# Kernel tuning notes

Measured on AMD Instinct MI355X. Metric: run time of the kernel, lower is better.

Reference implementation:

```python
import jax, jax.numpy as jnp
import numpy as np

G, P = 512, 128            # graphs, nodes per graph
NT, NL, NC = 120, 4, 4     # tracks/leptons/cells per graph (disjoint node targets)
W_NODE, W_BCE, W_F1 = 1.0, 1.0, 1.0  # config['loss weights']


def setup_inputs() -> dict:
    key = jax.random.key(0)
    ks = jax.random.split(key, 8)
    N = G * P
    T, L, C = G * NT, G * NL, G * NC
    E = G * P * P
    local = np.arange(P)[None, :] + (np.arange(G)[:, None] * P)  # [G,P] global node ids
    track_dst = jnp.asarray(local[:, :NT].ravel(), jnp.int32)
    lep_dst = jnp.asarray(local[:, NT:NT + NL].ravel(), jnp.int32)
    cell_dst = jnp.asarray(local[:, NT + NL:].ravel(), jnp.int32)
    ii, jj = np.meshgrid(np.arange(P), np.arange(P), indexing='ij')
    off = (np.arange(G) * P)[:, None, None]
    edge_src = jnp.asarray((off + ii[None]).reshape(-1), jnp.int32)
    edge_dst = jnp.asarray((off + jj[None]).reshape(-1), jnp.int32)
    edge_gid = jnp.asarray(np.repeat(np.arange(G), P * P), jnp.int32)
    node_gid = jnp.asarray(np.repeat(np.arange(G), P), jnp.int32)
    return {
        'node_prediction': jax.random.normal(ks[0], (N, 5), jnp.float32),
        'edge_prediction': jax.random.normal(ks[1], (E,), jnp.float32),
        'ce_weight': jnp.ones((5,), jnp.float32),
        'track_labels': jax.random.randint(ks[2], (T,), 0, 5, jnp.int32),
        'track_vtx': jax.random.randint(ks[3], (T,), 0, 10, jnp.int32),
        'lep_labels': jax.random.randint(ks[4], (L,), 0, 5, jnp.int32),
        'lep_vtx': jax.random.randint(ks[5], (L,), 0, 10, jnp.int32),
        'cell_labels': jax.random.randint(ks[6], (C,), 0, 5, jnp.int32),
        'cell_vtx': jax.random.randint(ks[7], (C,), 0, 10, jnp.int32),
        'track_dst': track_dst,
        'lep_dst': lep_dst,
        'cell_dst': cell_dst,
        'edge_src': edge_src,
        'edge_dst': edge_dst,
        'edge_gid': edge_gid,
        'node_gid': node_gid,
    }


def reference(node_prediction, edge_prediction, ce_weight,
              track_labels, track_vtx, lep_labels, lep_vtx, cell_labels, cell_vtx,
              track_dst, lep_dst, cell_dst, edge_src, edge_dst, edge_gid, node_gid):
    N = node_prediction.shape[0]

    def scatter(track_v, lep_v, cell_v):  # copy_src + sum over 3 edge types
        out = jnp.zeros((N,), jnp.int32)
        out = out.at[track_dst].add(track_v)
        out = out.at[lep_dst].add(lep_v)
        out = out.at[cell_dst].add(cell_v)
        return out

    node_labels = scatter(track_labels, lep_labels, cell_labels)
    node_vtx = scatter(track_vtx, lep_vtx, cell_vtx)

    # node CrossEntropyLoss (weight=[1]*5, ignore_index=-1, reduction='none')
    logp = jax.nn.log_softmax(node_prediction, axis=-1)
    valid = node_labels != -1
    lab = jnp.clip(node_labels, 0, 4)
    ce = -jnp.take_along_axis(logp, lab[:, None], axis=-1)[:, 0] * ce_weight[lab]
    ce = jnp.where(valid, ce, 0.0)
    node_loss = jax.ops.segment_sum(ce, node_gid, num_segments=G).mean()

    # edge weights (EdgeWeightFunction) and labels (EdgeLabelFunction)
    src_lab = node_labels[edge_src]
    dst_lab = node_labels[edge_dst]
    cond = ((dst_lab == 3) | (dst_lab == 2)) & ((src_lab == 3) | (src_lab == 2))
    w = jnp.where(cond, 2.0, 1.0).astype(jnp.float32)
    y = (node_vtx[edge_src] == node_vtx[edge_dst]).astype(jnp.float32)

    x = edge_prediction
    # BCEWithLogits: log(1+e^x) - x*y
    bce = (jnp.logaddexp(0.0, x) - x * y) * w
    e_cnt = jax.ops.segment_sum(jnp.ones_like(x), edge_gid, num_segments=G)
    edge_bce = (jax.ops.segment_sum(bce, edge_gid, num_segments=G) / e_cnt).mean()

    yh = jax.nn.sigmoid(x)
    tp = jax.ops.segment_sum(yh * y * w, edge_gid, num_segments=G)
    fn = jax.ops.segment_sum((1.0 - yh) * y * w, edge_gid, num_segments=G)
    fp = jax.ops.segment_sum(yh * (1.0 - y) * w, edge_gid, num_segments=G)
    edge_f1 = -(2.0 * tp / (2.0 * tp + fp + fn + 1e-10)).mean()

    loss = node_loss * W_NODE + edge_bce * W_BCE + edge_f1 * W_F1
    return loss
```

## Files before the change

### kernel.cpp

```cpp
#include <hip/hip_runtime.h>
#include <math.h>

#define NG     512
#define NP     128
#define NTRK   120
#define NLEP   4
#define NCEL   4
#define EPG    (NP * NP)
#define NTHREADS 256
#define SPLIT  4
#define NBLK   (NG * SPLIT)
#define EPB    (EPG / SPLIT)
#define F4ITERS (EPB / (NTHREADS * 4))


__global__ __launch_bounds__(NTHREADS) void vfl_main(
    const float* __restrict__ node_pred,
    const float* __restrict__ edge_pred,
    const float* __restrict__ ce_weight,
    const int* __restrict__ track_labels, const int* __restrict__ track_vtx,
    const int* __restrict__ lep_labels,   const int* __restrict__ lep_vtx,
    const int* __restrict__ cell_labels,  const int* __restrict__ cell_vtx,
    float* __restrict__ gout)
{
    const int b = blockIdx.x;
    const int g = b >> 2;
    const int s = b & 3;
    const int t = threadIdx.x;

    __shared__ float s_edge[EPB];
    __shared__ int   s_pack[NP];
    __shared__ float s_red[4][4];
    __shared__ int   s_cnt[10][2];

    {
        const float* ep_base = edge_pred + (size_t)g * EPG + (size_t)s * EPB;
        const int wv = t >> 6;
        const int ln = t & 63;
        #pragma unroll
        for (int k = 0; k < 4; ++k) {
            const int c = (k << 2) + wv;
            const float* gsrc = ep_base + c * 256 + ln * 4;
            __builtin_amdgcn_global_load_lds(
                (const __attribute__((address_space(1))) void*)gsrc,
                (__attribute__((address_space(3))) void*)&s_edge[c * 256],
                16, 0, 0);
        }
    }

    if (t < 20) ((int*)s_cnt)[t] = 0;

    float ce = 0.0f;
    int vtx = 0, is23 = 0;
    if (t < NP) {
        int lab;
        if (t < NTRK) {
            lab = track_labels[g * NTRK + t];
            vtx = track_vtx  [g * NTRK + t];
        } else if (t < NTRK + NLEP) {
            const int u = t - NTRK;
            lab = lep_labels[g * NLEP + u];
            vtx = lep_vtx  [g * NLEP + u];
        } else {
            const int u = t - NTRK - NLEP;
            lab = cell_labels[g * NCEL + u];
            vtx = cell_vtx  [g * NCEL + u];
        }
        is23 = (lab == 2 || lab == 3) ? 1 : 0;
        s_pack[t] = (vtx & 0xff) | (is23 << 8);

        if ((t >> 5) == s) {
            const float* np = node_pred + (size_t)(g * NP + t) * 5;
            const float x0 = np[0], x1 = np[1], x2 = np[2], x3 = np[3], x4 = np[4];
            const float m  = fmaxf(fmaxf(fmaxf(x0, x1), fmaxf(x2, x3)), x4);
            const float sm = __expf(x0 - m) + __expf(x1 - m) + __expf(x2 - m)
                           + __expf(x3 - m) + __expf(x4 - m);
            const float lse = m + __logf(sm);
            const float xl = (lab == 0) ? x0 : (lab == 1) ? x1 : (lab == 2) ? x2
                           : (lab == 3) ? x3 : x4;
            ce = (lse - xl) * ce_weight[lab];
        }
    }

    asm volatile("s_waitcnt vmcnt(0)" ::: "memory");
    __syncthreads();

    if (s == 0 && t < NP) atomicAdd(&s_cnt[vtx][is23], 1);

    const int j0 = (t & 31) << 2;
    const int pj0 = s_pack[j0 + 0];
    const int pj1 = s_pack[j0 + 1];
    const int pj2 = s_pack[j0 + 2];
    const int pj3 = s_pack[j0 + 3];
    const int ibase = s * 32 + (t >> 5);

    const float4* se4 = (const float4*)s_edge;

    float bce = 0.0f, swyh = 0.0f, tp = 0.0f;

    #pragma unroll
    for (int k = 0; k < F4ITERS; ++k) {
        const float4 v  = se4[k * NTHREADS + t];
        const int    pi = s_pack[ibase + k * 8];

        const float xs[4]  = { v.x, v.y, v.z, v.w };
        const int   pjs[4] = { pj0, pj1, pj2, pj3 };
        #pragma unroll
        for (int c = 0; c < 4; ++c) {
            const float x   = xs[c];
            const int   pjc = pjs[c];
            const bool  same = (((pi ^ pjc) & 0xff) == 0);
            const float w   = ((pi & pjc) & 0x100) ? 2.0f : 1.0f;
            const float wf  = same ? w : 0.0f;
            const float e  = __expf(-fabsf(x));
            const float t1 = 1.0f + e;
            const float r  = __builtin_amdgcn_rcpf(t1);
            const float sp = fmaxf(x, 0.0f) + __logf(t1);
            const float yh = (x >= 0.0f) ? r : (1.0f - r);
            bce  = fmaf(w,  sp, bce);
            bce  = fmaf(wf, -x, bce);
            swyh = fmaf(w,  yh, swyh);
            tp   = fmaf(wf, yh, tp);
        }
    }

    float vals[4] = { ce, bce, swyh, tp };
    #pragma unroll
    for (int i = 0; i < 4; ++i) {
        float x = vals[i];
        #pragma unroll
        for (int off = 32; off > 0; off >>= 1)
            x += __shfl_xor(x, off, 64);
        vals[i] = x;
    }
    const int wave = t >> 6;
    const int lane = t & 63;
    if (lane == 0) {
        #pragma unroll
        for (int i = 0; i < 4; ++i) s_red[wave][i] = vals[i];
    }
    __syncthreads();

    if (t == 0) {
        #pragma unroll
        for (int i = 0; i < 4; ++i)
            gout[i * NBLK + b] = s_red[0][i] + s_red[1][i] + s_red[2][i] + s_red[3][i];
        if (s == 0) {
            int swfy = 0;
            #pragma unroll
            for (int vv = 0; vv < 10; ++vv) {
                const int n0 = s_cnt[vv][0], n1 = s_cnt[vv][1];
                const int nt = n0 + n1;
                swfy += nt * nt + n1 * n1;
            }
            gout[4 * NBLK + b] = (float)swfy;
        }
    }
}

__global__ __launch_bounds__(256) void vfl_finalize(
    const float* __restrict__ gout, float* __restrict__ out)
{
    const int t = threadIdx.x;
    float ce = 0.0f, bce = 0.0f, f1 = 0.0f;
    for (int g2 = t; g2 < NG; g2 += 256) {
        float gce = 0.0f, gbce = 0.0f, gswyh = 0.0f, gtp = 0.0f;
        #pragma unroll
        for (int q = 0; q < SPLIT; ++q) {
            const int idx = g2 * SPLIT + q;
            gce   += gout[0 * NBLK + idx];
            gbce  += gout[1 * NBLK + idx];
            gswyh += gout[2 * NBLK + idx];
            gtp   += gout[3 * NBLK + idx];
        }
        const float gswfy = gout[4 * NBLK + g2 * SPLIT];
        ce  += gce;
        bce += gbce;
        const float fn = gswfy - gtp;
        const float fp = gswyh - gtp;
        f1  += (2.0f * gtp) / (2.0f * gtp + fp + fn + 1e-10f);
    }
    #pragma unroll
    for (int off = 32; off > 0; off >>= 1) {
        ce  += __shfl_xor(ce,  off, 64);
        bce += __shfl_xor(bce, off, 64);
        f1  += __shfl_xor(f1,  off, 64);
    }
    __shared__ float sred[4][3];
    const int wave = t >> 6;
    const int lane = t & 63;
    if (lane == 0) { sred[wave][0] = ce; sred[wave][1] = bce; sred[wave][2] = f1; }
    __syncthreads();
    if (t == 0) {
        const float tce  = sred[0][0] + sred[1][0] + sred[2][0] + sred[3][0];
        const float tbce = sred[0][1] + sred[1][1] + sred[2][1] + sred[3][1];
        const float tf1  = sred[0][2] + sred[1][2] + sred[2][2] + sred[3][2];
        out[0] = tce * (1.0f / NG)
               + tbce * (1.0f / ((float)NG * (float)EPG))
               - tf1 * (1.0f / NG);
    }
}

extern "C" void kernel_launch(void* const* d_in, const int* in_sizes, int n_in,
                              void* d_out, int out_size, void* d_ws, size_t ws_size,
                              hipStream_t stream)
{
    const float* node_pred    = (const float*)d_in[0];
    const float* edge_pred    = (const float*)d_in[1];
    const float* ce_weight    = (const float*)d_in[2];
    const int*   track_labels = (const int*)d_in[3];
    const int*   track_vtx    = (const int*)d_in[4];
    const int*   lep_labels   = (const int*)d_in[5];
    const int*   lep_vtx      = (const int*)d_in[6];
    const int*   cell_labels  = (const int*)d_in[7];
    const int*   cell_vtx     = (const int*)d_in[8];

    float* gout = (float*)d_ws;
    float* out  = (float*)d_out;

    vfl_main<<<NBLK, NTHREADS, 0, stream>>>(
        node_pred, edge_pred, ce_weight,
        track_labels, track_vtx, lep_labels, lep_vtx, cell_labels, cell_vtx,
        gout);
    vfl_finalize<<<1, 256, 0, stream>>>(gout, out);
}
```

Measured before the change: 20.90 us.

## Use one 1024-thread block per graph and compute per-graph loss in-block

Each graph is now handled by a single 1024-thread block holding the full 64KB edge tile in LDS, replacing four 256-thread blocks per graph. Per-graph CE, BCE and F1 are combined inside the block, so the finalize kernel only sums 512 scalars. This removes the cross-block partial writes and the heavier finalize pass. The trade-off is fewer, larger blocks with 64KB of LDS each, which may lower occupancy and latency hiding.

```diff
diff --git a/kernel.cpp b/kernel.cpp
--- a/kernel.cpp
+++ b/kernel.cpp
@@ -7,12 +7,8 @@
 #define NLEP   4
 #define NCEL   4
 #define EPG    (NP * NP)
-#define NTHREADS 256
-#define SPLIT  4
-#define NBLK   (NG * SPLIT)
-#define EPB    (EPG / SPLIT)
-#define F4ITERS (EPB / (NTHREADS * 4))
-
+#define NTHREADS 1024
+#define F4ITERS (EPG / (NTHREADS * 4))
 
 __global__ __launch_bounds__(NTHREADS) void vfl_main(
     const float* __restrict__ node_pred,
@@ -23,23 +19,21 @@
     const int* __restrict__ cell_labels,  const int* __restrict__ cell_vtx,
     float* __restrict__ gout)
 {
-    const int b = blockIdx.x;
-    const int g = b >> 2;
-    const int s = b & 3;
+    const int g = blockIdx.x;
     const int t = threadIdx.x;
+    const int wv = t >> 6;
+    const int ln = t & 63;
 
-    __shared__ float s_edge[EPB];
+    __shared__ float s_edge[EPG];
     __shared__ int   s_pack[NP];
-    __shared__ float s_red[4][4];
+    __shared__ float s_red[16][4];
     __shared__ int   s_cnt[10][2];
 
     {
-        const float* ep_base = edge_pred + (size_t)g * EPG + (size_t)s * EPB;
-        const int wv = t >> 6;
-        const int ln = t & 63;
+        const float* ep_base = edge_pred + (size_t)g * EPG;
         #pragma unroll
         for (int k = 0; k < 4; ++k) {
-            const int c = (k << 2) + wv;
+            const int c = (k << 4) + wv;
             const float* gsrc = ep_base + c * 256 + ln * 4;
             __builtin_amdgcn_global_load_lds(
                 (const __attribute__((address_space(1))) void*)gsrc,
@@ -69,30 +63,28 @@
         is23 = (lab == 2 || lab == 3) ? 1 : 0;
         s_pack[t] = (vtx & 0xff) | (is23 << 8);
 
-        if ((t >> 5) == s) {
-            const float* np = node_pred + (size_t)(g * NP + t) * 5;
-            const float x0 = np[0], x1 = np[1], x2 = np[2], x3 = np[3], x4 = np[4];
-            const float m  = fmaxf(fmaxf(fmaxf(x0, x1), fmaxf(x2, x3)), x4);
-            const float sm = __expf(x0 - m) + __expf(x1 - m) + __expf(x2 - m)
-                           + __expf(x3 - m) + __expf(x4 - m);
-            const float lse = m + __logf(sm);
-            const float xl = (lab == 0) ? x0 : (lab == 1) ? x1 : (lab == 2) ? x2
-                           : (lab == 3) ? x3 : x4;
-            ce = (lse - xl) * ce_weight[lab];
-        }
+        const float* np = node_pred + (size_t)(g * NP + t) * 5;
+        const float x0 = np[0], x1 = np[1], x2 = np[2], x3 = np[3], x4 = np[4];
+        const float m  = fmaxf(fmaxf(fmaxf(x0, x1), fmaxf(x2, x3)), x4);
+        const float sm = __expf(x0 - m) + __expf(x1 - m) + __expf(x2 - m)
+                       + __expf(x3 - m) + __expf(x4 - m);
+        const float lse = m + __logf(sm);
+        const float xl = (lab == 0) ? x0 : (lab == 1) ? x1 : (lab == 2) ? x2
+                       : (lab == 3) ? x3 : x4;
+        ce = (lse - xl) * ce_weight[lab];
     }
 
     asm volatile("s_waitcnt vmcnt(0)" ::: "memory");
     __syncthreads();
 
-    if (s == 0 && t < NP) atomicAdd(&s_cnt[vtx][is23], 1);
+    if (t < NP) atomicAdd(&s_cnt[vtx][is23], 1);
 
     const int j0 = (t & 31) << 2;
     const int pj0 = s_pack[j0 + 0];
     const int pj1 = s_pack[j0 + 1];
     const int pj2 = s_pack[j0 + 2];
     const int pj3 = s_pack[j0 + 3];
-    const int ibase = s * 32 + (t >> 5);
+    const int ibase = t >> 5;
 
     const float4* se4 = (const float4*)s_edge;
 
@@ -101,7 +93,7 @@
     #pragma unroll
     for (int k = 0; k < F4ITERS; ++k) {
         const float4 v  = se4[k * NTHREADS + t];
-        const int    pi = s_pack[ibase + k * 8];
+        const int    pi = s_pack[ibase + k * 32];
 
         const float xs[4]  = { v.x, v.y, v.z, v.w };
         const int   pjs[4] = { pj0, pj1, pj2, pj3 };
@@ -133,19 +125,24 @@
             x += __shfl_xor(x, off, 64);
         vals[i] = x;
     }
-    const int wave = t >> 6;
-    const int lane = t & 63;
-    if (lane == 0) {
+    if (ln == 0) {
         #pragma unroll
-        for (int i = 0; i < 4; ++i) s_red[wave][i] = vals[i];
+        for (int i = 0; i < 4; ++i) s_red[wv][i] = vals[i];
     }
     __syncthreads();
 
-    if (t == 0) {
+    if (t < 64) {
+        float x[4];
         #pragma unroll
         for (int i = 0; i < 4; ++i)
-            gout[i * NBLK + b] = s_red[0][i] + s_red[1][i] + s_red[2][i] + s_red[3][i];
-        if (s == 0) {
+            x[i] = (t < 16) ? s_red[t][i] : 0.0f;
+        #pragma unroll
+        for (int i = 0; i < 4; ++i) {
+            #pragma unroll
+            for (int off = 32; off > 0; off >>= 1)
+                x[i] += __shfl_xor(x[i], off, 64);
+        }
+        if (t == 0) {
             int swfy = 0;
             #pragma unroll
             for (int vv = 0; vv < 10; ++vv) {
@@ -153,7 +150,11 @@
                 const int nt = n0 + n1;
                 swfy += nt * nt + n1 * n1;
             }
-            gout[4 * NBLK + b] = (float)swfy;
+            const float gce = x[0], gbce = x[1], gswyh = x[2], gtp = x[3];
+            const float fn = (float)swfy - gtp;
+            const float fp = gswyh - gtp;
+            const float f1 = (2.0f * gtp) / (2.0f * gtp + fp + fn + 1e-10f);
+            gout[g] = gce + gbce * (1.0f / (float)EPG) - f1;
         }
     }
 }
@@ -162,43 +163,15 @@
     const float* __restrict__ gout, float* __restrict__ out)
 {
     const int t = threadIdx.x;
-    float ce = 0.0f, bce = 0.0f, f1 = 0.0f;
-    for (int g2 = t; g2 < NG; g2 += 256) {
-        float gce = 0.0f, gbce = 0.0f, gswyh = 0.0f, gtp = 0.0f;
-        #pragma unroll
-        for (int q = 0; q < SPLIT; ++q) {
-            const int idx = g2 * SPLIT + q;
-            gce   += gout[0 * NBLK + idx];
-            gbce  += gout[1 * NBLK + idx];
-            gswyh += gout[2 * NBLK + idx];
-            gtp   += gout[3 * NBLK + idx];
-        }
-        const float gswfy = gout[4 * NBLK + g2 * SPLIT];
-        ce  += gce;
-        bce += gbce;
-        const float fn = gswfy - gtp;
-        const float fp = gswyh - gtp;
-        f1  += (2.0f * gtp) / (2.0f * gtp + fp + fn + 1e-10f);
-    }
+    float acc = gout[t] + gout[t + 256];
     #pragma unroll
-    for (int off = 32; off > 0; off >>= 1) {
-        ce  += __shfl_xor(ce,  off, 64);
-        bce += __shfl_xor(bce, off, 64);
-        f1  += __shfl_xor(f1,  off, 64);
-    }
-    __shared__ float sred[4][3];
-    const int wave = t >> 6;
-    const int lane = t & 63;
-    if (lane == 0) { sred[wave][0] = ce; sred[wave][1] = bce; sred[wave][2] = f1; }
+    for (int off = 32; off > 0; off >>= 1)
+        acc += __shfl_xor(acc, off, 64);
+    __shared__ float sred[4];
+    if ((t & 63) == 0) sred[t >> 6] = acc;
     __syncthreads();
-    if (t == 0) {
-        const float tce  = sred[0][0] + sred[1][0] + sred[2][0] + sred[3][0];
-        const float tbce = sred[0][1] + sred[1][1] + sred[2][1] + sred[3][1];
-        const float tf1  = sred[0][2] + sred[1][2] + sred[2][2] + sred[3][2];
-        out[0] = tce * (1.0f / NG)
-               + tbce * (1.0f / ((float)NG * (float)EPG))
-               - tf1 * (1.0f / NG);
-    }
+    if (t == 0)
+        out[0] = (sred[0] + sred[1] + sred[2] + sred[3]) * (1.0f / NG);
 }
 
 extern "C" void kernel_launch(void* const* d_in, const int* in_sizes, int n_in,
@@ -211,14 +184,14 @@
     const int*   track_labels = (const int*)d_in[3];
     const int*   track_vtx    = (const int*)d_in[4];
     const int*   lep_labels   = (const int*)d_in[5];
-    const int*   lep_vtx      = (const int*)d_in[6];
+    const int*   lep_vtx     = (const int*)d_in[6];
     const int*   cell_labels  = (const int*)d_in[7];
-    const int*   cell_vtx     = (const int*)d_in[8];
+    const int*   cell_vtx    = (const int*)d_in[8];
 
     float* gout = (float*)d_ws;
     float* out  = (float*)d_out;
 
-    vfl_main<<<NBLK, NTHREADS, 0, stream>>>(
+    vfl_main<<<NG, NTHREADS, 0, stream>>>(
         node_pred, edge_pred, ce_weight,
         track_labels, track_vtx, lep_labels, lep_vtx, cell_labels, cell_vtx,
         gout);
```

Result: faster. 18.45 us (-11.7%).
